# Kernel optimization log

Measured on AMD Instinct MI355X. Metric: run time of the kernel, lower is better.

## Reference

```python
import jax, jax.numpy as jnp
import numpy as np

K_SCOPE = 25.0
K_ENV = 100.0
K_LABEL_4 = 1.5
WIN = int(K_SCOPE) + 2
N = 65536
H = W = 4096


def setup_inputs() -> dict:
    key = jax.random.key(0)
    k1, k2, k3, k4 = jax.random.split(key, 4)
    # positions well inside the map so windows stay (mostly) in bounds
    first_frame = jax.random.uniform(k1, (N, 2), minval=64.0, maxval=H - 64.0)
    current_step = jax.random.normal(k2, (N, 2)) * 5.0
    current_vel = jax.random.normal(k3, (N, 2))
    semantic_map = jax.random.randint(k4, (H, W), 0, 6).astype(jnp.int32)
    F0 = jnp.zeros((N, 2), jnp.float32)
    return {"current_step": current_step, "first_frame": first_frame,
            "current_vel": current_vel, "semantic_map": semantic_map, "F0": F0}


def reference(current_step, first_frame, current_vel, semantic_map, F0):
    Hm, Wm = semantic_map.shape
    ori = current_step + first_frame                      # [N,2]
    scope = ori + jnp.sign(current_vel) * K_SCOPE
    a0 = jnp.floor(ori).astype(jnp.int32)                 # (r0,c0)
    a1 = jnp.floor(scope).astype(jnp.int32)               # (r1,c1)
    r0, c0 = a0[:, 0], a0[:, 1]
    r1, c1 = a1[:, 0], a1[:, 1]
    rmin, rmax = jnp.minimum(r0, r1), jnp.maximum(r0, r1)
    cmin, cmax = jnp.minimum(c0, c1), jnp.maximum(c0, c1)
    deg_r = r0 == r1
    deg_c = c0 == c1

    lr = jnp.arange(WIN)
    lc = jnp.arange(WIN)
    rows = rmin[:, None] + lr[None, :]
    cols = cmin[:, None] + lc[None, :]
    rin = (rows >= 0) & (rows < Hm)
    cin = (cols >= 0) & (cols < Wm)
    # gathered per-agent windows anchored at the region's min corner
    win = semantic_map[jnp.clip(rows, 0, Hm - 1)[:, :, None],
                       jnp.clip(cols, 0, Wm - 1)[:, None, :]]

    # region mask: degenerate axis -> single line at local index 0; else half-open extent
    mr = jnp.where(deg_r[:, None], lr[None, :] == 0, lr[None, :] < (rmax - rmin)[:, None])
    mc = jnp.where(deg_c[:, None], lc[None, :] == 0, lc[None, :] < (cmax - cmin)[:, None])
    both_deg = deg_r & deg_c
    mask = (mr & rin)[:, :, None] & (mc & cin)[:, None, :] & (~both_deg)[:, None, None]

    lr_f = lr.astype(jnp.float32)
    lc_f = lc.astype(jnp.float32)

    def force_for_label(label, weight, plus_one_row):
        match = (mask & (win == label)).astype(jnp.float32)
        cnt = jnp.sum(match, axis=(1, 2))                     # [N]
        denom = jnp.maximum(cnt, 1.0)
        mean_r = jnp.einsum('nrc,r->n', match, lr_f) / denom  # local-coord centroid
        mean_c = jnp.einsum('nrc,c->n', match, lc_f) / denom

        def safe(d):
            return jnp.where(d == 0, 1.0, d)

        # Case A: same row, cols differ (1D horizontal slice)
        disA = jnp.where(c0 < c1, mean_c, K_SCOPE - mean_c)
        dirA = jnp.where((c0 < c1)[:, None], jnp.array([0.0, -1.0]), jnp.array([0.0, 1.0]))
        FA = (weight * K_ENV / safe(disA))[:, None] * dirA
        FA = jnp.where((disA != 0)[:, None], FA, 0.0)

        # Case B: same col, rows differ (1D vertical slice); label-5 quirk adds +1
        disB = jnp.where(r0 < r1, mean_r + plus_one_row, K_SCOPE - mean_r)
        dirB = jnp.where((r0 < r1)[:, None], jnp.array([-1.0, 0.0]), jnp.array([1.0, 0.0]))
        FB = (weight * K_ENV / safe(disB))[:, None] * dirB
        FB = jnp.where((disB != 0)[:, None], FB, 0.0)

        # Case C: full 2D region, force from the corner matching travel direction
        corner = jnp.stack([jnp.where(r0 < r1, 0.0, K_SCOPE),
                            jnp.where(c0 < c1, 0.0, K_SCOPE)], axis=1)   # [N,2]
        obstacle = jnp.stack([mean_r, mean_c], axis=1)
        d = obstacle - corner
        disC = jnp.sqrt(jnp.sum(d * d, axis=1))
        FC = -(weight * K_ENV) * d / (safe(disC) ** 2)[:, None]
        FC = jnp.where((disC != 0)[:, None], FC, 0.0)

        F = jnp.where((deg_r & ~deg_c)[:, None], FA,
                      jnp.where((~deg_r & deg_c)[:, None], FB, FC))
        active = (cnt > 0) & (~both_deg)
        return jnp.where(active[:, None], F, 0.0)

    F2 = jnp.zeros_like(F0)
    F2 = F2 + force_for_label(5, 1.0, 1.0)        # label 5: +1 row-distance quirk
    F2 = F2 + force_for_label(3, 1.0, 0.0)        # label 3
    F2 = F2 + force_for_label(4, K_LABEL_4, 0.0)  # label 4, scaled by k_label_4
    return F2
```

## Files before the change

kernel.cpp:

```cpp
#include <hip/hip_runtime.h>
#include <math.h>

#define HM 4096
#define WM 4096

struct AgentGeom {
    int r0, c0, r1, c1;
    int rmin, cmin;
    int nr, nc;
    bool deg_r, deg_c, both;
};

__device__ __forceinline__ AgentGeom agent_geom(const float* __restrict__ cstep,
                                                const float* __restrict__ fframe,
                                                const float* __restrict__ cvel, int n)
{
    AgentGeom g;
    const float ori_r = cstep[2*n+0] + fframe[2*n+0];
    const float ori_c = cstep[2*n+1] + fframe[2*n+1];
    const float vr = cvel[2*n+0], vc = cvel[2*n+1];
    const float sgr = (vr > 0.f) ? 1.f : ((vr < 0.f) ? -1.f : 0.f);
    const float sgc = (vc > 0.f) ? 1.f : ((vc < 0.f) ? -1.f : 0.f);
    g.r0 = (int)floorf(ori_r);
    g.c0 = (int)floorf(ori_c);
    g.r1 = (int)floorf(ori_r + sgr * 25.0f);
    g.c1 = (int)floorf(ori_c + sgc * 25.0f);
    g.rmin = min(g.r0, g.r1);
    g.cmin = min(g.c0, g.c1);
    g.deg_r = (g.r0 == g.r1);
    g.deg_c = (g.c0 == g.c1);
    g.both  = g.deg_r && g.deg_c;
    g.nr = g.deg_r ? 1 : min(max(g.r0, g.r1) - g.rmin, 27);
    g.nc = g.deg_c ? 1 : min(max(g.c0, g.c1) - g.cmin, 27);
    return g;
}

__device__ __forceinline__ void force_from_counts(const AgentGeom& g,
    const int cnts[3], const int srs[3], const int scs[3], float& Fr, float& Fc)
{
    const float wts[3] = {1.0f, 1.0f, 1.5f};
    const float p1s[3] = {1.0f, 0.0f, 0.0f};
    Fr = 0.0f; Fc = 0.0f;
    #pragma unroll
    for (int i = 0; i < 3; ++i) {
        const float denom  = fmaxf((float)cnts[i], 1.0f);
        const float mean_r = (float)srs[i] / denom;
        const float mean_c = (float)scs[i] / denom;
        float fr, fc;
        if (g.deg_r && !g.deg_c) {
            const float disA = (g.c0 < g.c1) ? mean_c : (25.0f - mean_c);
            const float mag  = (disA != 0.0f) ? (wts[i] * 100.0f / disA) : 0.0f;
            fr = 0.0f;
            fc = (g.c0 < g.c1) ? -mag : mag;
        } else if (!g.deg_r && g.deg_c) {
            const float disB = (g.r0 < g.r1) ? (mean_r + p1s[i]) : (25.0f - mean_r);
            const float mag  = (disB != 0.0f) ? (wts[i] * 100.0f / disB) : 0.0f;
            fr = (g.r0 < g.r1) ? -mag : mag;
            fc = 0.0f;
        } else {
            const float crn_r = (g.r0 < g.r1) ? 0.0f : 25.0f;
            const float crn_c = (g.c0 < g.c1) ? 0.0f : 25.0f;
            const float dr = mean_r - crn_r;
            const float dc = mean_c - crn_c;
            const float disC = sqrtf(dr * dr + dc * dc);
            if (disC != 0.0f) {
                const float s = -(wts[i] * 100.0f) / (disC * disC);
                fr = s * dr; fc = s * dc;
            } else { fr = 0.0f; fc = 0.0f; }
        }
        if (cnts[i] > 0 && !g.both) { Fr += fr; Fc += fc; }
    }
}

__global__ __launch_bounds__(256) void nsp_gather(
    const float* __restrict__ cstep, const float* __restrict__ fframe,
    const float* __restrict__ cvel, const int* __restrict__ smap,
    int* __restrict__ ws, float* __restrict__ out, int fused, int N)
{
    const int wave = (blockIdx.x * blockDim.x + threadIdx.x) >> 6;
    const int lane = threadIdx.x & 63;
    const int half = lane >> 5;
    const int l5   = lane & 31;
    const int n    = wave * 2 + half;
    const bool live = (n < N);
    const int n_eff = live ? n : (N - 1);

    const AgentGeom g = agent_geom(cstep, fframe, cvel, n_eff);

    const int cg  = l5 & 7;
    const int rho = l5 >> 3;
    const int a   = g.cmin & ~3;
    const int d   = g.cmin - a;

    unsigned B = 0;
    #pragma unroll
    for (int k = 0; k < 4; ++k) {
        const int wc  = cg * 4 + k - d;
        const int col = a + cg * 4 + k;
        const bool bad = ((unsigned)wc >= (unsigned)g.nc) ||
                         ((unsigned)col >= (unsigned)WM);
        B |= bad ? (0xFFu << (8 * k)) : 0u;
    }

    const int T_half = (g.nr + 3) >> 2;
    const int t_lane = (rho < g.nr) ? ((g.nr - rho + 3) >> 2) : 0;
    const int T_oth  = __shfl_xor(T_half, 32);
    const int T_wave = max(T_half, T_oth);

    const bool fastl = (g.rmin >= 0) && (g.rmin + 28 <= HM) &&
                       (a >= 0) && (a + 32 <= WM);
    const bool fastw = __all(fastl ? 1 : 0);

    unsigned W5 = 0, S5 = 0, W3 = 0, S3 = 0, W4 = 0, S4 = 0;
    const unsigned k01 = 0x01010101u;

    if (fastw) {
        const int lane_off = rho * WM + a + cg * 4;
        for (int j = 0; j < T_wave; ++j) {
            const int4 v = *reinterpret_cast<const int4*>(
                smap + (size_t)((g.rmin + 4 * j) * WM + lane_off));
            unsigned y = ((((((unsigned)v.w << 8) | (unsigned)v.z) << 8)
                           | (unsigned)v.y) << 8) | (unsigned)v.x;
            y |= B;
            y = (j < t_lane) ? y : 0xFFFFFFFFu;
            const unsigned b1 = y >> 1, b2 = y >> 2;
            const unsigned m5 = ( y & ~b1 &  b2) & k01;
            const unsigned m3 = ( y &  b1 & ~b2) & k01;
            const unsigned m4 = (~y & ~b1 &  b2) & k01;
            W5 += m5; S5 += W5;
            W3 += m3; S3 += W3;
            W4 += m4; S4 += W4;
        }
    } else {
        for (int j = 0; j < T_wave; ++j) {
            const int rrow = g.rmin + rho + 4 * j;
            const int rcl  = min(max(rrow, 0), HM - 1);
            unsigned y = 0;
            #pragma unroll
            for (int k = 0; k < 4; ++k) {
                const int col  = a + cg * 4 + k;
                const int colc = min(max(col, 0), WM - 1);
                const unsigned vv = (unsigned)smap[(size_t)rcl * WM + colc];
                y |= vv << (8 * k);
            }
            y |= B;
            const bool rok = (j < t_lane) && ((unsigned)rrow < (unsigned)HM);
            y = rok ? y : 0xFFFFFFFFu;
            const unsigned b1 = y >> 1, b2 = y >> 2;
            const unsigned m5 = ( y & ~b1 &  b2) & k01;
            const unsigned m3 = ( y &  b1 & ~b2) & k01;
            const unsigned m4 = (~y & ~b1 &  b2) & k01;
            W5 += m5; S5 += W5;
            W3 += m3; S3 += W3;
            W4 += m4; S4 += W4;
        }
    }

    #define BYTESUM(x) ((int)(((x) * 0x01010101u) >> 24))
    const int c5 = BYTESUM(W5), c3 = BYTESUM(W3), c4 = BYTESUM(W4);
    const int rs5 = rho * c5 + 4 * (T_wave * c5 - BYTESUM(S5));
    const int rs3 = rho * c3 + 4 * (T_wave * c3 - BYTESUM(S3));
    const int rs4 = rho * c4 + 4 * (T_wave * c4 - BYTESUM(S4));
    #define KSUM(W) ((int)(((W) >> 8) & 0xFFu) + 2 * (int)(((W) >> 16) & 0xFFu) + 3 * (int)((W) >> 24))
    const int cbase = cg * 4 - d;
    const int cs5 = cbase * c5 + KSUM(W5);
    const int cs3 = cbase * c3 + KSUM(W3);
    const int cs4v = cbase * c4 + KSUM(W4);

    unsigned q5 = (unsigned)c5 | ((unsigned)rs5 << 10);
    unsigned q3 = (unsigned)c3 | ((unsigned)rs3 << 10);
    unsigned q4 = (unsigned)c4 | ((unsigned)rs4 << 10);
    unsigned scp = (unsigned)cs5 | ((unsigned)cs3 << 15);
    int      sc4 = cs4v;

    #pragma unroll
    for (int o = 1; o <= 16; o <<= 1) {
        q5  += __shfl_xor(q5, o);
        q3  += __shfl_xor(q3, o);
        q4  += __shfl_xor(q4, o);
        scp += __shfl_xor(scp, o);
        sc4 += __shfl_xor(sc4, o);
    }

    if (l5 == 0 && live) {
        if (!fused) {
            int4* w4 = reinterpret_cast<int4*>(ws + (size_t)n * 8);
            *w4 = make_int4((int)q5, (int)q3, (int)q4, (int)scp);
            ws[(size_t)n * 8 + 4] = sc4;
        } else {
            const int cnts[3] = {(int)(q5 & 1023u), (int)(q3 & 1023u), (int)(q4 & 1023u)};
            const int srs[3]  = {(int)(q5 >> 10),   (int)(q3 >> 10),   (int)(q4 >> 10)};
            const int scs[3]  = {(int)(scp & 0x7FFFu), (int)(scp >> 15), sc4};
            float Fr, Fc;
            force_from_counts(g, cnts, srs, scs, Fr, Fc);
            out[2*n+0] = Fr;
            out[2*n+1] = Fc;
        }
    }
}

__global__ __launch_bounds__(256) void nsp_force(
    const float* __restrict__ cstep, const float* __restrict__ fframe,
    const float* __restrict__ cvel, const int* __restrict__ ws,
    float* __restrict__ out, int N)
{
    const int n = blockIdx.x * blockDim.x + threadIdx.x;
    if (n >= N) return;
    const AgentGeom g = agent_geom(cstep, fframe, cvel, n);
    const int4 w4 = *reinterpret_cast<const int4*>(ws + (size_t)n * 8);
    const int sc4 = ws[(size_t)n * 8 + 4];
    const unsigned q5 = (unsigned)w4.x, q3 = (unsigned)w4.y,
                   q4 = (unsigned)w4.z, scp = (unsigned)w4.w;
    const int cnts[3] = {(int)(q5 & 1023u), (int)(q3 & 1023u), (int)(q4 & 1023u)};
    const int srs[3]  = {(int)(q5 >> 10),   (int)(q3 >> 10),   (int)(q4 >> 10)};
    const int scs[3]  = {(int)(scp & 0x7FFFu), (int)(scp >> 15), sc4};
    float Fr, Fc;
    force_from_counts(g, cnts, srs, scs, Fr, Fc);
    out[2*n+0] = Fr;
    out[2*n+1] = Fc;
}

extern "C" void kernel_launch(void* const* d_in, const int* in_sizes, int n_in,
                              void* d_out, int out_size, void* d_ws, size_t ws_size,
                              hipStream_t stream) {
    const float* cstep  = (const float*)d_in[0];
    const float* fframe = (const float*)d_in[1];
    const float* cvel   = (const float*)d_in[2];
    const int*   smap   = (const int*)d_in[3];
    float* out = (float*)d_out;
    int*   ws  = (int*)d_ws;

    const int N = in_sizes[0] / 2;
    const bool fused = (ws == nullptr) || (ws_size < (size_t)N * 8 * sizeof(int));

    const int waves  = (N + 1) / 2;
    const int blocks = (waves * 64 + 255) / 256;
    hipLaunchKernelGGL(nsp_gather, dim3(blocks), dim3(256), 0, stream,
                       cstep, fframe, cvel, smap, ws, out, fused ? 1 : 0, N);
    if (!fused) {
        hipLaunchKernelGGL(nsp_force, dim3((N + 255) / 256), dim3(256), 0, stream,
                           cstep, fframe, cvel, ws, out, N);
    }
}
```

Measured before the change: 149.9 us.

## Pack semantic map to bytes and bin agents by tile before gathering

Adds a prep kernel that packs the int32 semantic map into a byte map in workspace, then bins agents into 256x256 spatial tiles with a histogram, scan and scatter to build a permutation. The gather kernel walks agents in tile order, reads 4-byte words from the byte map, and remaps block IDs across 8 groups (likely targeting XCD locality). This is meant to cut gather traffic and improve cache locality. The cost is a full 64MB read pass over the map plus four extra launches with atomics, which may outweigh the savings for 65536 agents.

After: 194.4 us. 1.3x slower.

```diff
diff --git a/kernel.cpp b/kernel.cpp
--- a/kernel.cpp
+++ b/kernel.cpp
@@ -3,6 +3,8 @@
 
 #define HM 4096
 #define WM 4096
+
+#define WS_HIST_OFF 4194304
 
 struct AgentGeom {
     int r0, c0, r1, c1;
@@ -72,10 +74,201 @@
     }
 }
 
-__global__ __launch_bounds__(256) void nsp_gather(
+__device__ __forceinline__ int agent_tile(const float* __restrict__ cstep,
+                                          const float* __restrict__ fframe, int n)
+{
+    const float orr = cstep[2*n+0] + fframe[2*n+0];
+    const float occ = cstep[2*n+1] + fframe[2*n+1];
+    const int r = min(max((int)floorf(orr), 0), HM - 1);
+    const int c = min(max((int)floorf(occ), 0), WM - 1);
+    return ((r >> 8) << 4) | (c >> 8);
+}
+
+__global__ __launch_bounds__(256) void nsp_prep(
+    const int* __restrict__ smap, uint4* __restrict__ bmap4, int* __restrict__ hist)
+{
+    if (blockIdx.x == 0 && threadIdx.x < 512) hist[threadIdx.x] = 0;
+    const int total16 = (HM * WM) / 16;
+    const int stride  = gridDim.x * blockDim.x;
+    for (int i = blockIdx.x * blockDim.x + threadIdx.x; i < total16; i += stride) {
+        const int4* src = reinterpret_cast<const int4*>(smap) + (size_t)i * 4;
+        const int4 v0 = src[0], v1 = src[1], v2 = src[2], v3 = src[3];
+        const unsigned o0 = (unsigned)v0.x | ((unsigned)v0.y << 8) | ((unsigned)v0.z << 16) | ((unsigned)v0.w << 24);
+        const unsigned o1 = (unsigned)v1.x | ((unsigned)v1.y << 8) | ((unsigned)v1.z << 16) | ((unsigned)v1.w << 24);
+        const unsigned o2 = (unsigned)v2.x | ((unsigned)v2.y << 8) | ((unsigned)v2.z << 16) | ((unsigned)v2.w << 24);
+        const unsigned o3 = (unsigned)v3.x | ((unsigned)v3.y << 8) | ((unsigned)v3.z << 16) | ((unsigned)v3.w << 24);
+        bmap4[i] = make_uint4(o0, o1, o2, o3);
+    }
+}
+
+__global__ __launch_bounds__(256) void nsp_hist(
+    const float* __restrict__ cstep, const float* __restrict__ fframe,
+    int* __restrict__ hist, int N)
+{
+    const int n = blockIdx.x * blockDim.x + threadIdx.x;
+    if (n >= N) return;
+    atomicAdd(&hist[agent_tile(cstep, fframe, n)], 1);
+}
+
+__global__ __launch_bounds__(64) void nsp_scan(int* __restrict__ hist)
+{
+    const int lane = threadIdx.x;
+    const int h0 = hist[lane*4+0], h1 = hist[lane*4+1];
+    const int h2 = hist[lane*4+2], h3 = hist[lane*4+3];
+    const int tot = h0 + h1 + h2 + h3;
+    int inc = tot;
+    #pragma unroll
+    for (int o = 1; o < 64; o <<= 1) {
+        const int v = __shfl_up(inc, o);
+        if (lane >= o) inc += v;
+    }
+    const int base = inc - tot;
+    int* cursor = hist + 256;
+    cursor[lane*4+0] = base;
+    cursor[lane*4+1] = base + h0;
+    cursor[lane*4+2] = base + h0 + h1;
+    cursor[lane*4+3] = base + h0 + h1 + h2;
+}
+
+__global__ __launch_bounds__(256) void nsp_scatter(
+    const float* __restrict__ cstep, const float* __restrict__ fframe,
+    int* __restrict__ cursor, int* __restrict__ perm, int N)
+{
+    const int n = blockIdx.x * blockDim.x + threadIdx.x;
+    if (n >= N) return;
+    const int pos = atomicAdd(&cursor[agent_tile(cstep, fframe, n)], 1);
+    perm[pos] = n;
+}
+
+__global__ __launch_bounds__(256) void nsp_gather_b(
+    const float* __restrict__ cstep, const float* __restrict__ fframe,
+    const float* __restrict__ cvel, const unsigned char* __restrict__ bmap,
+    const int* __restrict__ perm, float* __restrict__ out, int N)
+{
+    const int nb  = gridDim.x;
+    int bid = blockIdx.x;
+    if ((nb & 7) == 0) {
+        const int cpx = nb >> 3;
+        bid = (bid & 7) * cpx + (bid >> 3);
+    }
+    const int wave = bid * 4 + (int)(threadIdx.x >> 6);
+    const int lane = threadIdx.x & 63;
+    const int half = lane >> 5;
+    const int l5   = lane & 31;
+    const int idx  = wave * 2 + half;
+    const bool live = (idx < N);
+    const int n = perm[live ? idx : (N - 1)];
+
+    const AgentGeom g = agent_geom(cstep, fframe, cvel, n);
+
+    const int cg  = l5 & 7;
+    const int rho = l5 >> 3;
+    const int a   = g.cmin & ~3;
+    const int d   = g.cmin - a;
+
+    unsigned B = 0;
+    #pragma unroll
+    for (int k = 0; k < 4; ++k) {
+        const int wc  = cg * 4 + k - d;
+        const int col = a + cg * 4 + k;
+        const bool bad = ((unsigned)wc >= (unsigned)g.nc) ||
+                         ((unsigned)col >= (unsigned)WM);
+        B |= bad ? (0xFFu << (8 * k)) : 0u;
+    }
+
+    const int T_half = (g.nr + 3) >> 2;
+    const int t_lane = (rho < g.nr) ? ((g.nr - rho + 3) >> 2) : 0;
+    const int T_oth  = __shfl_xor(T_half, 32);
+    const int T_wave = max(T_half, T_oth);
+
+    const bool fastl = (g.rmin >= 0) && (g.rmin + 28 <= HM) &&
+                       (a >= 0) && (a + 32 <= WM);
+    const bool fastw = __all(fastl ? 1 : 0);
+
+    unsigned W5 = 0, S5 = 0, W3 = 0, S3 = 0, W4 = 0, S4 = 0;
+    const unsigned k01 = 0x01010101u;
+
+    if (fastw) {
+        const unsigned char* p = bmap + (size_t)(g.rmin + rho) * WM + a + cg * 4;
+        #pragma unroll 2
+        for (int j = 0; j < T_wave; ++j) {
+            unsigned y = *reinterpret_cast<const unsigned*>(p);
+            p += 4 * WM;
+            y |= B;
+            y = (j < t_lane) ? y : 0xFFFFFFFFu;
+            const unsigned b1 = y >> 1, b2 = y >> 2;
+            const unsigned m5 = ( y & ~b1 &  b2) & k01;
+            const unsigned m3 = ( y &  b1 & ~b2) & k01;
+            const unsigned m4 = (~y & ~b1 &  b2) & k01;
+            W5 += m5; S5 += W5;
+            W3 += m3; S3 += W3;
+            W4 += m4; S4 += W4;
+        }
+    } else {
+        for (int j = 0; j < T_wave; ++j) {
+            const int rrow = g.rmin + rho + 4 * j;
+            const int rcl  = min(max(rrow, 0), HM - 1);
+            unsigned y = 0;
+            #pragma unroll
+            for (int k = 0; k < 4; ++k) {
+                const int col  = a + cg * 4 + k;
+                const int colc = min(max(col, 0), WM - 1);
+                y |= ((unsigned)bmap[(size_t)rcl * WM + colc]) << (8 * k);
+            }
+            y |= B;
+            const bool rok = (j < t_lane) && ((unsigned)rrow < (unsigned)HM);
+            y = rok ? y : 0xFFFFFFFFu;
+            const unsigned b1 = y >> 1, b2 = y >> 2;
+            const unsigned m5 = ( y & ~b1 &  b2) & k01;
+            const unsigned m3 = ( y &  b1 & ~b2) & k01;
+            const unsigned m4 = (~y & ~b1 &  b2) & k01;
+            W5 += m5; S5 += W5;
+            W3 += m3; S3 += W3;
+            W4 += m4; S4 += W4;
+        }
+    }
+
+    #define BYTESUM(x) ((int)(((x) * 0x01010101u) >> 24))
+    const int c5 = BYTESUM(W5), c3 = BYTESUM(W3), c4 = BYTESUM(W4);
+    const int rs5 = rho * c5 + 4 * (T_wave * c5 - BYTESUM(S5));
+    const int rs3 = rho * c3 + 4 * (T_wave * c3 - BYTESUM(S3));
+    const int rs4 = rho * c4 + 4 * (T_wave * c4 - BYTESUM(S4));
+    #define KSUM(W) ((int)(((W) >> 8) & 0xFFu) + 2 * (int)(((W) >> 16) & 0xFFu) + 3 * (int)((W) >> 24))
+    const int cbase = cg * 4 - d;
+    const int cs5 = cbase * c5 + KSUM(W5);
+    const int cs3 = cbase * c3 + KSUM(W3);
+    const int cs4v = cbase * c4 + KSUM(W4);
+
+    unsigned q5 = (unsigned)c5 | ((unsigned)rs5 << 10);
+    unsigned q3 = (unsigned)c3 | ((unsigned)rs3 << 10);
+    unsigned q4 = (unsigned)c4 | ((unsigned)rs4 << 10);
+    unsigned scp = (unsigned)cs5 | ((unsigned)cs3 << 15);
+    int      sc4 = cs4v;
+
+    #pragma unroll
+    for (int o = 1; o <= 16; o <<= 1) {
+        q5  += __shfl_xor(q5, o);
+        q3  += __shfl_xor(q3, o);
+        q4  += __shfl_xor(q4, o);
+        scp += __shfl_xor(scp, o);
+        sc4 += __shfl_xor(sc4, o);
+    }
+
+    if (l5 == 0 && live) {
+        const int cnts[3] = {(int)(q5 & 1023u), (int)(q3 & 1023u), (int)(q4 & 1023u)};
+        const int srs[3]  = {(int)(q5 >> 10),   (int)(q3 >> 10),   (int)(q4 >> 10)};
+        const int scs[3]  = {(int)(scp & 0x7FFFu), (int)(scp >> 15), sc4};
+        float Fr, Fc;
+        force_from_counts(g, cnts, srs, scs, Fr, Fc);
+        out[2*n+0] = Fr;
+        out[2*n+1] = Fc;
+    }
+}
+
+__global__ __launch_bounds__(256) void nsp_gather_int(
     const float* __restrict__ cstep, const float* __restrict__ fframe,
     const float* __restrict__ cvel, const int* __restrict__ smap,
-    int* __restrict__ ws, float* __restrict__ out, int fused, int N)
+    float* __restrict__ out, int N)
 {
     const int wave = (blockIdx.x * blockDim.x + threadIdx.x) >> 6;
     const int lane = threadIdx.x & 63;
@@ -140,8 +333,7 @@
             for (int k = 0; k < 4; ++k) {
                 const int col  = a + cg * 4 + k;
                 const int colc = min(max(col, 0), WM - 1);
-                const unsigned vv = (unsigned)smap[(size_t)rcl * WM + colc];
-                y |= vv << (8 * k);
+                y |= ((unsigned)smap[(size_t)rcl * WM + colc]) << (8 * k);
             }
             y |= B;
             const bool rok = (j < t_lane) && ((unsigned)rrow < (unsigned)HM);
@@ -156,12 +348,10 @@
         }
     }
 
-    #define BYTESUM(x) ((int)(((x) * 0x01010101u) >> 24))
     const int c5 = BYTESUM(W5), c3 = BYTESUM(W3), c4 = BYTESUM(W4);
     const int rs5 = rho * c5 + 4 * (T_wave * c5 - BYTESUM(S5));
     const int rs3 = rho * c3 + 4 * (T_wave * c3 - BYTESUM(S3));
     const int rs4 = rho * c4 + 4 * (T_wave * c4 - BYTESUM(S4));
-    #define KSUM(W) ((int)(((W) >> 8) & 0xFFu) + 2 * (int)(((W) >> 16) & 0xFFu) + 3 * (int)((W) >> 24))
     const int cbase = cg * 4 - d;
     const int cs5 = cbase * c5 + KSUM(W5);
     const int cs3 = cbase * c3 + KSUM(W3);
@@ -183,41 +373,14 @@
     }
 
     if (l5 == 0 && live) {
-        if (!fused) {
-            int4* w4 = reinterpret_cast<int4*>(ws + (size_t)n * 8);
-            *w4 = make_int4((int)q5, (int)q3, (int)q4, (int)scp);
-            ws[(size_t)n * 8 + 4] = sc4;
-        } else {
-            const int cnts[3] = {(int)(q5 & 1023u), (int)(q3 & 1023u), (int)(q4 & 1023u)};
-            const int srs[3]  = {(int)(q5 >> 10),   (int)(q3 >> 10),   (int)(q4 >> 10)};
-            const int scs[3]  = {(int)(scp & 0x7FFFu), (int)(scp >> 15), sc4};
-            float Fr, Fc;
-            force_from_counts(g, cnts, srs, scs, Fr, Fc);
-            out[2*n+0] = Fr;
-            out[2*n+1] = Fc;
-        }
-    }
-}
-
-__global__ __launch_bounds__(256) void nsp_force(
-    const float* __restrict__ cstep, const float* __restrict__ fframe,
-    const float* __restrict__ cvel, const int* __restrict__ ws,
-    float* __restrict__ out, int N)
-{
-    const int n = blockIdx.x * blockDim.x + threadIdx.x;
-    if (n >= N) return;
-    const AgentGeom g = agent_geom(cstep, fframe, cvel, n);
-    const int4 w4 = *reinterpret_cast<const int4*>(ws + (size_t)n * 8);
-    const int sc4 = ws[(size_t)n * 8 + 4];
-    const unsigned q5 = (unsigned)w4.x, q3 = (unsigned)w4.y,
-                   q4 = (unsigned)w4.z, scp = (unsigned)w4.w;
-    const int cnts[3] = {(int)(q5 & 1023u), (int)(q3 & 1023u), (int)(q4 & 1023u)};
-    const int srs[3]  = {(int)(q5 >> 10),   (int)(q3 >> 10),   (int)(q4 >> 10)};
-    const int scs[3]  = {(int)(scp & 0x7FFFu), (int)(scp >> 15), sc4};
-    float Fr, Fc;
-    force_from_counts(g, cnts, srs, scs, Fr, Fc);
-    out[2*n+0] = Fr;
-    out[2*n+1] = Fc;
+        const int cnts[3] = {(int)(q5 & 1023u), (int)(q3 & 1023u), (int)(q4 & 1023u)};
+        const int srs[3]  = {(int)(q5 >> 10),   (int)(q3 >> 10),   (int)(q4 >> 10)};
+        const int scs[3]  = {(int)(scp & 0x7FFFu), (int)(scp >> 15), sc4};
+        float Fr, Fc;
+        force_from_counts(g, cnts, srs, scs, Fr, Fc);
+        out[2*n+0] = Fr;
+        out[2*n+1] = Fc;
+    }
 }
 
 extern "C" void kernel_launch(void* const* d_in, const int* in_sizes, int n_in,
@@ -228,17 +391,32 @@
     const float* cvel   = (const float*)d_in[2];
     const int*   smap   = (const int*)d_in[3];
     float* out = (float*)d_out;
-    int*   ws  = (int*)d_ws;
 
     const int N = in_sizes[0] / 2;
-    const bool fused = (ws == nullptr) || (ws_size < (size_t)N * 8 * sizeof(int));
-
-    const int waves  = (N + 1) / 2;
-    const int blocks = (waves * 64 + 255) / 256;
-    hipLaunchKernelGGL(nsp_gather, dim3(blocks), dim3(256), 0, stream,
-                       cstep, fframe, cvel, smap, ws, out, fused ? 1 : 0, N);
-    if (!fused) {
-        hipLaunchKernelGGL(nsp_force, dim3((N + 255) / 256), dim3(256), 0, stream,
-                           cstep, fframe, cvel, ws, out, N);
-    }
-}
+    const size_t need = (size_t)(WS_HIST_OFF + 512 + N) * sizeof(int);
+
+    if (d_ws != nullptr && ws_size >= need) {
+        unsigned char* bmap = (unsigned char*)d_ws;
+        int* hist   = (int*)d_ws + WS_HIST_OFF;
+        int* cursor = hist + 256;
+        int* perm   = hist + 512;
+
+        hipLaunchKernelGGL(nsp_prep, dim3(2048), dim3(256), 0, stream,
+                           smap, (uint4*)bmap, hist);
+        hipLaunchKernelGGL(nsp_hist, dim3((N + 255) / 256), dim3(256), 0, stream,
+                           cstep, fframe, hist, N);
+        hipLaunchKernelGGL(nsp_scan, dim3(1), dim3(64), 0, stream, hist);
+        hipLaunchKernelGGL(nsp_scatter, dim3((N + 255) / 256), dim3(256), 0, stream,
+                           cstep, fframe, cursor, perm, N);
+
+        const int waves  = (N + 1) / 2;
+        const int blocks = (waves + 3) / 4;
+        hipLaunchKernelGGL(nsp_gather_b, dim3(blocks), dim3(256), 0, stream,
+                           cstep, fframe, cvel, bmap, perm, out, N);
+    } else {
+        const int waves  = (N + 1) / 2;
+        const int blocks = (waves * 64 + 255) / 256;
+        hipLaunchKernelGGL(nsp_gather_int, dim3(blocks), dim3(256), 0, stream,
+                           cstep, fframe, cvel, smap, out, N);
+    }
+}
```
